# Performance work log

Hardware: AMD Instinct MI355X
Metric: run time of the kernel (lower is better)

Reference implementation:

```python
import jax, jax.numpy as jnp
import numpy as np

NUM_ITEM = 80000
NUM_USER = 20000
N = NUM_ITEM + NUM_USER
E = 1_000_000
DIM_FEAT = 64
USER_DIM = 128
DIM_ID = 64
SLOPE = 0.01  # F.leaky_relu default negative_slope


def setup_inputs() -> dict:
    key = jax.random.key(0)
    ks = jax.random.split(key, 16)
    s = 0.05
    # self-loop-free random edge list (torch code removes self loops)
    src = jax.random.randint(ks[0], (E,), 0, N)
    off = jax.random.randint(ks[1], (E,), 1, N)
    dst = (src + off) % N
    edge_index = jnp.stack([src, dst]).astype(jnp.int32)
    return {
        "features": jax.random.normal(ks[2], (NUM_ITEM, DIM_FEAT), jnp.float32),
        "user_features": jax.random.normal(ks[3], (NUM_USER, USER_DIM), jnp.float32),
        "id_embedding_weight": jax.random.normal(ks[4], (N, DIM_ID), jnp.float32) * s,
        "user_mlp_w": jax.random.normal(ks[5], (DIM_FEAT, USER_DIM), jnp.float32) * s,
        "user_mlp_b": jnp.zeros((DIM_FEAT,), jnp.float32),
        "gat1_w": jax.random.normal(ks[6], (DIM_FEAT, DIM_FEAT), jnp.float32) * s,
        "lin1_w": jax.random.normal(ks[7], (DIM_ID, DIM_FEAT), jnp.float32) * s,
        "lin1_b": jnp.zeros((DIM_ID,), jnp.float32),
        "g1_w": jax.random.normal(ks[8], (DIM_ID, DIM_FEAT), jnp.float32) * s,
        "g1_b": jnp.zeros((DIM_ID,), jnp.float32),
        "gat2_w": jax.random.normal(ks[9], (DIM_ID, DIM_ID), jnp.float32) * s,
        "lin2_w": jax.random.normal(ks[10], (DIM_ID, DIM_ID), jnp.float32) * s,
        "lin2_b": jnp.zeros((DIM_ID,), jnp.float32),
        "g2_w": jax.random.normal(ks[11], (DIM_ID, DIM_ID), jnp.float32) * s,
        "g2_b": jnp.zeros((DIM_ID,), jnp.float32),
        "edge_index": edge_index,
    }


def leaky_relu(x):
    return jnp.where(x >= 0, x, SLOPE * x)


def graph_gat(x, W, src, dst):
    """GraphGAT layer (MGAT-style): x@W, inner-product attention with
    degree-based sigmoid gate, edge softmax over target nodes, scatter-add."""
    n = x.shape[0]
    xw = x @ W                                   # [N, d_out]
    x_i = xw[dst]                                # gathered target feats [E, d]
    x_j = xw[src]                                # gathered source feats [E, d]
    inner = jnp.sum(x_i * x_j, axis=-1)          # [E]
    deg = jnp.zeros((n,), xw.dtype).at[src].add(1.0)
    dinv = deg[src] ** -0.5                      # deg[src] >= 1 by construction
    gate = jax.nn.sigmoid(dinv * inner)
    logits = inner * gate
    # segment softmax over destination index (PyG softmax)
    m = jax.ops.segment_max(logits, dst, num_segments=n)
    m = jnp.where(jnp.isfinite(m), m, 0.0)
    e = jnp.exp(logits - m[dst])
    z = jax.ops.segment_sum(e, dst, num_segments=n)
    attn = e / (z[dst] + 1e-16)
    msg = x_j * attn[:, None]                    # [E, d]
    return jnp.zeros_like(xw).at[dst].add(msg)   # scatter-add aggr


def reference(features, user_features, id_embedding_weight,
              user_mlp_w, user_mlp_b,
              gat1_w, lin1_w, lin1_b, g1_w, g1_b,
              gat2_w, lin2_w, lin2_b, g2_w, g2_b,
              edge_index):
    src, dst = edge_index[0], edge_index[1]
    user = jnp.tanh(user_features @ user_mlp_w.T + user_mlp_b)
    x = jnp.concatenate([features, user], axis=0)          # [N, dim_feat]
    nrm = jnp.linalg.norm(x, axis=-1, keepdims=True)
    x = x / jnp.maximum(nrm, 1e-12)                        # F.normalize

    # hop 1
    h = leaky_relu(graph_gat(x, gat1_w, src, dst))
    x_hat = leaky_relu(x @ lin1_w.T + lin1_b) + id_embedding_weight
    x1 = leaky_relu(h @ g1_w.T + g1_b + x_hat)

    # hop 2
    h = leaky_relu(graph_gat(x1, gat2_w, src, dst))
    x_hat = leaky_relu(x1 @ lin2_w.T + lin2_b) + id_embedding_weight
    x2 = leaky_relu(h @ g2_w.T + g2_b + x_hat)

    return jnp.concatenate([x1, x2], axis=1)               # [N, 2*dim_id]
```

## Files before the change

kernel.cpp:

```cpp
#include <hip/hip_runtime.h>
#include <hip/hip_bf16.h>

#define N_ITEM 80000
#define N_USER 20000
#define NN     100000
#define NE     1000000
#define SCAN_T 1024
#define SCAN_TILES ((NN + SCAN_T - 1) / SCAN_T)

typedef __hip_bfloat16 bf16;

__device__ __forceinline__ float b2f(bf16 v) { return __bfloat162float(v); }
__device__ __forceinline__ bf16  f2b(float v) { return __float2bfloat16(v); }
__device__ __forceinline__ float bits2f(unsigned short h) {
    return __uint_as_float(((unsigned)h) << 16);
}
__device__ __forceinline__ float leaky(float v) { return v >= 0.f ? v : 0.01f * v; }

template<typename T>
__device__ __forceinline__ float ldT(const void* p, size_t i);
template<> __device__ __forceinline__ float ldT<float>(const void* p, size_t i) {
    return ((const float*)p)[i];
}
template<> __device__ __forceinline__ float ldT<bf16>(const void* p, size_t i) {
    return b2f(((const bf16*)p)[i]);
}
template<typename T>
__device__ __forceinline__ float4 ldT4(const void* p, size_t i);
template<> __device__ __forceinline__ float4 ldT4<float>(const void* p, size_t i) {
    return *(const float4*)((const float*)p + i);
}
template<> __device__ __forceinline__ float4 ldT4<bf16>(const void* p, size_t i) {
    ushort4 u = *(const ushort4*)((const unsigned short*)p + i);
    return make_float4(bits2f(u.x), bits2f(u.y), bits2f(u.z), bits2f(u.w));
}
template<typename T>
__device__ __forceinline__ void stT4(void* p, size_t i, float4 v);
template<> __device__ __forceinline__ void stT4<float>(void* p, size_t i, float4 v) {
    *(float4*)((float*)p + i) = v;
}
template<> __device__ __forceinline__ void stT4<bf16>(void* p, size_t i, float4 v) {
    bf16 b0 = f2b(v.x), b1 = f2b(v.y), b2 = f2b(v.z), b3 = f2b(v.w);
    ushort4 u = make_ushort4(*(unsigned short*)&b0, *(unsigned short*)&b1,
                             *(unsigned short*)&b2, *(unsigned short*)&b3);
    *(ushort4*)((unsigned short*)p + i) = u;
}
__device__ __forceinline__ float4 ld4f(const float* p, size_t i) {
    return *(const float4*)(p + i);
}

__device__ __forceinline__ float wred(float v) {
    for (int o = 32; o; o >>= 1) v += __shfl_xor(v, o, 64);
    return v;
}
__device__ __forceinline__ float gred16(float v) {
    for (int o = 8; o; o >>= 1) v += __shfl_xor(v, o, 64);
    return v;
}
__device__ __forceinline__ int wscan(int v, int lane) {
    for (int o = 1; o < 64; o <<= 1) {
        int t = __shfl_up(v, o, 64);
        v += (lane >= o) ? t : 0;
    }
    return v;
}

__global__ void k_detect(const unsigned short* __restrict__ w, int* __restrict__ mode) {
    __shared__ int cnt[256];
    int bad = 0;
    for (int i = threadIdx.x; i < 4096; i += 256) {
        unsigned e = (w[i] >> 7) & 0xFFu;
        bad += (e == 0u || e == 0xFFu) ? 1 : 0;
    }
    cnt[threadIdx.x] = bad;
    __syncthreads();
    if (threadIdx.x == 0) {
        int t = 0;
        for (int k = 0; k < 256; k++) t += cnt[k];
        mode[0] = (t > 0) ? 1 : 0;
    }
}

__global__ void k_prep_w(const void* umw, const void* lw1, const void* gw1,
                         const void* lw2, const void* gw2,
                         float* umwT, float* wT, const int* mode) {
    int t = blockIdx.x * 256 + threadIdx.x;
    bool f32m = (*mode != 0);
    if (t < 8192) {
        int j = t >> 7, k = t & 127;
        float v = f32m ? ldT<float>(umw, t) : ldT<bf16>(umw, t);
        umwT[k * 64 + j] = v;
    } else {
        int u = t - 8192;
        int m = u >> 12;
        int r = u & 4095;
        int j = r >> 6, k = r & 63;
        const void* srcp = (m == 0) ? lw1 : (m == 1) ? gw1 : (m == 2) ? lw2 : gw2;
        float v = f32m ? ldT<float>(srcp, r) : ldT<bf16>(srcp, r);
        wT[m * 4096 + k * 64 + j] = v;
    }
}

__global__ void k_deg(const int* __restrict__ src, const int* __restrict__ dst,
                      int* __restrict__ deg, int* __restrict__ cnt) {
    int e = blockIdx.x * blockDim.x + threadIdx.x;
    if (e < NE) {
        atomicAdd(&deg[src[e]], 1);
        atomicAdd(&cnt[dst[e]], 1);
    }
}

__global__ void k_scan_sum(const int* __restrict__ cnt, int* __restrict__ tsum) {
    __shared__ int wsum[16];
    int i = blockIdx.x * SCAN_T + threadIdx.x;
    int lane = threadIdx.x & 63, wid = threadIdx.x >> 6;
    int v = (i < NN) ? cnt[i] : 0;
    float s = wred((float)v);
    if (lane == 0) wsum[wid] = (int)s;
    __syncthreads();
    if (threadIdx.x == 0) {
        int t = 0;
        #pragma unroll
        for (int k = 0; k < 16; k++) t += wsum[k];
        tsum[blockIdx.x] = t;
    }
}

__global__ void k_scan_tiles(const int* __restrict__ tsum, int* __restrict__ toff) {
    __shared__ int wsum[16];
    int lane = threadIdx.x & 63, wid = threadIdx.x >> 6;
    int v = (threadIdx.x < SCAN_TILES) ? tsum[threadIdx.x] : 0;
    int inc = wscan(v, lane);
    if (lane == 63) wsum[wid] = inc;
    __syncthreads();
    if (wid == 0) {
        int ws = (lane < 16) ? wsum[lane] : 0;
        int wi = wscan(ws, lane);
        if (lane < 16) wsum[lane] = wi - ws;
    }
    __syncthreads();
    if (threadIdx.x < SCAN_TILES) toff[threadIdx.x] = inc - v + wsum[wid];
}

__global__ void k_scan_out(const int* __restrict__ cnt, const int* __restrict__ toff,
                           int* __restrict__ csr_off, int* __restrict__ cursor) {
    __shared__ int wsum[16];
    int i = blockIdx.x * SCAN_T + threadIdx.x;
    int lane = threadIdx.x & 63, wid = threadIdx.x >> 6;
    int v = (i < NN) ? cnt[i] : 0;
    int inc = wscan(v, lane);
    if (lane == 63) wsum[wid] = inc;
    __syncthreads();
    if (wid == 0) {
        int ws = (lane < 16) ? wsum[lane] : 0;
        int wi = wscan(ws, lane);
        if (lane < 16) wsum[lane] = wi - ws;
    }
    __syncthreads();
    int excl = inc - v + wsum[wid] + toff[blockIdx.x];
    if (i < NN) { csr_off[i] = excl; cursor[i] = excl; }
    if (i == NN - 1) csr_off[NN] = excl + v;
}

__global__ void k_scatter(const int* __restrict__ src, const int* __restrict__ dst,
                          int* __restrict__ cursor, int* __restrict__ csr_src) {
    int e = blockIdx.x * blockDim.x + threadIdx.x;
    if (e < NE) {
        int pos = atomicAdd(&cursor[dst[e]], 1);
        csr_src[pos] = src[e];
    }
}

template<typename T>
__device__ __forceinline__ void prep_items_body(const void* feat, float* x) {
    int i = blockIdx.x * 4 + (threadIdx.x >> 6);
    int j = threadIdx.x & 63;
    if (i >= N_ITEM) return;
    float v = ldT<T>(feat, (size_t)i * 64 + j);
    float ss = wred(v * v);
    float inv = 1.f / fmaxf(sqrtf(ss), 1e-12f);
    x[(size_t)i * 64 + j] = v * inv;
}
__global__ void k_prep_items(const void* feat, float* x, const int* mode) {
    if (*mode) prep_items_body<float>(feat, x);
    else       prep_items_body<bf16>(feat, x);
}

template<typename T>
__device__ __forceinline__ void prep_users_body(const void* uf, const float* wT,
                                                const void* b, float* x) {
    int u = blockIdx.x * 4 + (threadIdx.x >> 6);
    int j = threadIdx.x & 63;
    if (u >= N_USER) return;
    size_t ub = (size_t)u * 128;
    float acc = ldT<T>(b, j);
    #pragma unroll 8
    for (int k = 0; k < 128; k++)
        acc += ldT<T>(uf, ub + k) * wT[k * 64 + j];
    float v = tanhf(acc);
    float ss = wred(v * v);
    float inv = 1.f / fmaxf(sqrtf(ss), 1e-12f);
    x[(size_t)(N_ITEM + u) * 64 + j] = v * inv;
}
__global__ void k_prep_users(const void* uf, const float* wT, const void* b,
                             float* x, const int* mode) {
    if (*mode) prep_users_body<float>(uf, wT, b, x);
    else       prep_users_body<bf16>(uf, wT, b, x);
}

template<typename T>
__device__ __forceinline__ void xw_body(const float* __restrict__ xin,
                                        const void* __restrict__ W,
                                        float* __restrict__ xw) {
    int lane = threadIdx.x & 63, wid = threadIdx.x >> 6;
    int sl = lane & 15;
    int i = blockIdx.x * 16 + (wid << 2) + (lane >> 4);
    if (i >= NN) return;
    size_t rb = (size_t)i * 64 + sl * 4;
    float4 xv = ld4f(xin, rb);
    float4 acc = make_float4(0.f, 0.f, 0.f, 0.f);
    int gbase = lane & 48;
    #pragma unroll
    for (int kk = 0; kk < 16; kk++) {
        int srcl = gbase | kk;
        float xb[4];
        xb[0] = __shfl(xv.x, srcl, 64);
        xb[1] = __shfl(xv.y, srcl, 64);
        xb[2] = __shfl(xv.z, srcl, 64);
        xb[3] = __shfl(xv.w, srcl, 64);
        #pragma unroll
        for (int q = 0; q < 4; q++) {
            float4 w4 = ldT4<T>(W, (size_t)(kk * 4 + q) * 64 + sl * 4);
            acc.x += xb[q] * w4.x; acc.y += xb[q] * w4.y;
            acc.z += xb[q] * w4.z; acc.w += xb[q] * w4.w;
        }
    }
    *(float4*)(xw + rb) = acc;
}
__global__ void k_xw(const float* xin, const void* W, float* xw, const int* mode) {
    if (*mode) xw_body<float>(xin, W, xw);
    else       xw_body<bf16>(xin, W, xw);
}

template<typename T>
__device__ __forceinline__ void gat_body(const float* __restrict__ xw,
                                         const float* __restrict__ xin,
                                         const int* __restrict__ csr_off,
                                         const int* __restrict__ csr_src,
                                         const int* __restrict__ deg,
                                         const float* __restrict__ gT, const void* gb,
                                         const float* __restrict__ lT, const void* lb,
                                         const void* id_emb,
                                         float* __restrict__ xnext, void* out,
                                         int off_out) {
    int lane = threadIdx.x & 63, wid = threadIdx.x >> 6;
    int sl = lane & 15;
    int i = blockIdx.x * 16 + (wid << 2) + (lane >> 4);
    if (i >= NN) return;
    size_t rb = (size_t)i * 64 + sl * 4;
    float4 xd = ld4f(xw, rb);
    int e0 = csr_off[i], e1 = csr_off[i + 1];
    int cnt = e1 - e0;
    float m = -1e30f, l = 0.f;
    float4 acc = make_float4(0.f, 0.f, 0.f, 0.f);
    float4 xsP = make_float4(0.f, 0.f, 0.f, 0.f);
    float dP = 1.f;
    if (cnt > 0) {
        int s0 = csr_src[e0];
        xsP = ld4f(xw, (size_t)s0 * 64 + sl * 4);
        dP = (float)deg[s0];
    }
    for (int t = 0; t < cnt; ++t) {
        float4 xs = xsP; float dv = dP;
        if (t + 1 < cnt) {
            int sn = csr_src[e0 + t + 1];
            xsP = ld4f(xw, (size_t)sn * 64 + sl * 4);
            dP = (float)deg[sn];
        }
        float p = xd.x * xs.x + xd.y * xs.y + xd.z * xs.z + xd.w * xs.w;
        float inner = gred16(p);
        float gate = 1.f / (1.f + __expf(-rsqrtf(dv) * inner));
        float logit = inner * gate;
        float mn = fmaxf(m, logit);
        float sc = __expf(m - mn);
        float w  = __expf(logit - mn);
        acc.x = acc.x * sc + w * xs.x;
        acc.y = acc.y * sc + w * xs.y;
        acc.z = acc.z * sc + w * xs.z;
        acc.w = acc.w * sc + w * xs.w;
        l = l * sc + w;
        m = mn;
    }
    float linv = 1.f / (l + 1e-16f);
    float4 hv = make_float4(leaky(acc.x * linv), leaky(acc.y * linv),
                            leaky(acc.z * linv), leaky(acc.w * linv));
    float4 xv = ld4f(xin, rb);
    float4 accg = make_float4(0.f, 0.f, 0.f, 0.f);
    float4 accl = make_float4(0.f, 0.f, 0.f, 0.f);
    int gbase = lane & 48;
    #pragma unroll
    for (int kk = 0; kk < 16; kk++) {
        int srcl = gbase | kk;
        float hb[4], xb[4];
        hb[0] = __shfl(hv.x, srcl, 64); xb[0] = __shfl(xv.x, srcl, 64);
        hb[1] = __shfl(hv.y, srcl, 64); xb[1] = __shfl(xv.y, srcl, 64);
        hb[2] = __shfl(hv.z, srcl, 64); xb[2] = __shfl(xv.z, srcl, 64);
        hb[3] = __shfl(hv.w, srcl, 64); xb[3] = __shfl(xv.w, srcl, 64);
        #pragma unroll
        for (int q = 0; q < 4; q++) {
            size_t wb = (size_t)(kk * 4 + q) * 64 + sl * 4;
            float4 g4 = ld4f(gT, wb);
            float4 l4 = ld4f(lT, wb);
            accg.x += hb[q] * g4.x; accg.y += hb[q] * g4.y;
            accg.z += hb[q] * g4.z; accg.w += hb[q] * g4.w;
            accl.x += xb[q] * l4.x; accl.y += xb[q] * l4.y;
            accl.z += xb[q] * l4.z; accl.w += xb[q] * l4.w;
        }
    }
    float4 lb4 = ldT4<T>(lb, sl * 4);
    float4 gb4 = ldT4<T>(gb, sl * 4);
    float4 id4 = ldT4<T>(id_emb, rb);
    float4 xn;
    xn.x = leaky(accg.x + gb4.x + leaky(accl.x + lb4.x) + id4.x);
    xn.y = leaky(accg.y + gb4.y + leaky(accl.y + lb4.y) + id4.y);
    xn.z = leaky(accg.z + gb4.z + leaky(accl.z + lb4.z) + id4.z);
    xn.w = leaky(accg.w + gb4.w + leaky(accl.w + lb4.w) + id4.w);
    *(float4*)(xnext + rb) = xn;
    stT4<T>(out, (size_t)i * 128 + off_out + sl * 4, xn);
}
__global__ void k_gat(const float* xw, const float* xin,
                      const int* csr_off, const int* csr_src, const int* deg,
                      const float* gT, const void* gb,
                      const float* lT, const void* lb, const void* id_emb,
                      float* xnext, void* out, int off_out, const int* mode) {
    if (*mode) gat_body<float>(xw, xin, csr_off, csr_src, deg, gT, gb, lT, lb,
                               id_emb, xnext, out, off_out);
    else       gat_body<bf16>(xw, xin, csr_off, csr_src, deg, gT, gb, lT, lb,
                              id_emb, xnext, out, off_out);
}

extern "C" void kernel_launch(void* const* d_in, const int* in_sizes, int n_in,
                              void* d_out, int out_size, void* d_ws, size_t ws_size,
                              hipStream_t stream) {
    const void* feat   = d_in[0];
    const void* uf     = d_in[1];
    const void* id_emb = d_in[2];
    const void* umw    = d_in[3];
    const void* umb    = d_in[4];
    const void* gat1   = d_in[5];
    const void* lin1b  = d_in[7];
    const void* g1b    = d_in[9];
    const void* gat2   = d_in[10];
    const void* lin2b  = d_in[12];
    const void* g2b    = d_in[14];
    const int*  ei     = (const int*)d_in[15];
    const int* src = ei;
    const int* dst = ei + NE;

    int*      mode   = (int*)d_ws;
    int*      deg    = (int*)((char*)d_ws + 16);
    int*      cnt    = deg + NN;
    int*      cursor = cnt + NN;
    int*      csr_off = cursor + NN;
    int*      tsum   = csr_off + NN + 16;
    int*      toff   = tsum + 128;
    float*    umwT   = (float*)(toff + 128);
    float*    wT     = umwT + 8192;
    int*      csr_src = (int*)(wT + 4 * 4096);
    float*    buf0   = (float*)(csr_src + NE);
    float*    buf1   = buf0 + (size_t)NN * 64;
    float*    buf2   = buf1 + (size_t)NN * 64;

    k_detect<<<1, 256, 0, stream>>>((const unsigned short*)feat, mode);
    k_prep_w<<<96, 256, 0, stream>>>(umw, d_in[6], d_in[8], d_in[11], d_in[13],
                                     umwT, wT, mode);
    hipMemsetAsync(deg, 0, 2 * NN * 4, stream);
    k_deg<<<(NE + 255) / 256, 256, 0, stream>>>(src, dst, deg, cnt);
    k_scan_sum<<<SCAN_TILES, SCAN_T, 0, stream>>>(cnt, tsum);
    k_scan_tiles<<<1, SCAN_T, 0, stream>>>(tsum, toff);
    k_scan_out<<<SCAN_TILES, SCAN_T, 0, stream>>>(cnt, toff, csr_off, cursor);
    k_scatter<<<(NE + 255) / 256, 256, 0, stream>>>(src, dst, cursor, csr_src);
    k_prep_items<<<(N_ITEM + 3) / 4, 256, 0, stream>>>(feat, buf0, mode);
    k_prep_users<<<(N_USER + 3) / 4, 256, 0, stream>>>(uf, umwT, umb, buf0, mode);

    const float* lT1 = wT;
    const float* gT1 = wT + 4096;
    const float* lT2 = wT + 8192;
    const float* gT2 = wT + 12288;

    int gat_blocks = (NN + 15) / 16;

    k_xw<<<gat_blocks, 256, 0, stream>>>(buf0, gat1, buf1, mode);
    k_gat<<<gat_blocks, 256, 0, stream>>>(buf1, buf0, csr_off, csr_src, deg,
                                          gT1, g1b, lT1, lin1b, id_emb,
                                          buf2, d_out, 0, mode);
    k_xw<<<gat_blocks, 256, 0, stream>>>(buf2, gat2, buf1, mode);
    k_gat<<<gat_blocks, 256, 0, stream>>>(buf1, buf2, csr_off, csr_src, deg,
                                          gT2, g2b, lT2, lin2b, id_emb,
                                          buf0, d_out, 64, mode);
}
```

Baseline: 698.2 us.

## Store xW in bf16, precompute inverse sqrt degree, deepen gather prefetch

The projected features xW are now stored as bf16 instead of fp32, which halves the bytes the GAT kernel gathers per edge in its random neighbour loop. A new small kernel computes rsqrt(degree) once per node, so the edge loop reads a ready float instead of converting and taking rsqrt per edge. The software prefetch in the edge loop now runs two neighbours ahead instead of one, to hide more gather latency. The cost is bf16 rounding of the attention inputs, which may reduce accuracy, plus one extra tiny launch and some extra registers.

```diff
diff --git a/kernel.cpp b/kernel.cpp
--- a/kernel.cpp
+++ b/kernel.cpp
@@ -47,6 +47,16 @@
 }
 __device__ __forceinline__ float4 ld4f(const float* p, size_t i) {
     return *(const float4*)(p + i);
+}
+__device__ __forceinline__ float4 ld4b(const unsigned short* p, size_t i) {
+    ushort4 u = *(const ushort4*)(p + i);
+    return make_float4(bits2f(u.x), bits2f(u.y), bits2f(u.z), bits2f(u.w));
+}
+__device__ __forceinline__ void st4b(unsigned short* p, size_t i, float4 v) {
+    bf16 b0 = f2b(v.x), b1 = f2b(v.y), b2 = f2b(v.z), b3 = f2b(v.w);
+    ushort4 u = make_ushort4(*(unsigned short*)&b0, *(unsigned short*)&b1,
+                             *(unsigned short*)&b2, *(unsigned short*)&b3);
+    *(ushort4*)(p + i) = u;
 }
 
 __device__ __forceinline__ float wred(float v) {
@@ -110,6 +120,11 @@
     }
 }
 
+__global__ void k_dinv(const int* __restrict__ deg, float* __restrict__ dinv) {
+    int i = blockIdx.x * blockDim.x + threadIdx.x;
+    if (i < NN) dinv[i] = rsqrtf((float)max(deg[i], 1));
+}
+
 __global__ void k_scan_sum(const int* __restrict__ cnt, int* __restrict__ tsum) {
     __shared__ int wsum[16];
     int i = blockIdx.x * SCAN_T + threadIdx.x;
@@ -211,7 +226,7 @@
 template<typename T>
 __device__ __forceinline__ void xw_body(const float* __restrict__ xin,
                                         const void* __restrict__ W,
-                                        float* __restrict__ xw) {
+                                        unsigned short* __restrict__ xw) {
     int lane = threadIdx.x & 63, wid = threadIdx.x >> 6;
     int sl = lane & 15;
     int i = blockIdx.x * 16 + (wid << 2) + (lane >> 4);
@@ -235,19 +250,20 @@
             acc.z += xb[q] * w4.z; acc.w += xb[q] * w4.w;
         }
     }
-    *(float4*)(xw + rb) = acc;
-}
-__global__ void k_xw(const float* xin, const void* W, float* xw, const int* mode) {
+    st4b(xw, rb, acc);
+}
+__global__ void k_xw(const float* xin, const void* W, unsigned short* xw,
+                     const int* mode) {
     if (*mode) xw_body<float>(xin, W, xw);
     else       xw_body<bf16>(xin, W, xw);
 }
 
 template<typename T>
-__device__ __forceinline__ void gat_body(const float* __restrict__ xw,
+__device__ __forceinline__ void gat_body(const unsigned short* __restrict__ xw,
                                          const float* __restrict__ xin,
                                          const int* __restrict__ csr_off,
                                          const int* __restrict__ csr_src,
-                                         const int* __restrict__ deg,
+                                         const float* __restrict__ dinv,
                                          const float* __restrict__ gT, const void* gb,
                                          const float* __restrict__ lT, const void* lb,
                                          const void* id_emb,
@@ -258,28 +274,34 @@
     int i = blockIdx.x * 16 + (wid << 2) + (lane >> 4);
     if (i >= NN) return;
     size_t rb = (size_t)i * 64 + sl * 4;
-    float4 xd = ld4f(xw, rb);
+    float4 xd = ld4b(xw, rb);
     int e0 = csr_off[i], e1 = csr_off[i + 1];
     int cnt = e1 - e0;
     float m = -1e30f, l = 0.f;
     float4 acc = make_float4(0.f, 0.f, 0.f, 0.f);
-    float4 xsP = make_float4(0.f, 0.f, 0.f, 0.f);
-    float dP = 1.f;
+    float4 xsA = make_float4(0.f, 0.f, 0.f, 0.f), xsB = xsA;
+    float dA = 1.f, dB = 1.f;
     if (cnt > 0) {
         int s0 = csr_src[e0];
-        xsP = ld4f(xw, (size_t)s0 * 64 + sl * 4);
-        dP = (float)deg[s0];
+        xsA = ld4b(xw, (size_t)s0 * 64 + sl * 4);
+        dA = dinv[s0];
+    }
+    if (cnt > 1) {
+        int s1 = csr_src[e0 + 1];
+        xsB = ld4b(xw, (size_t)s1 * 64 + sl * 4);
+        dB = dinv[s1];
     }
     for (int t = 0; t < cnt; ++t) {
-        float4 xs = xsP; float dv = dP;
-        if (t + 1 < cnt) {
-            int sn = csr_src[e0 + t + 1];
-            xsP = ld4f(xw, (size_t)sn * 64 + sl * 4);
-            dP = (float)deg[sn];
+        float4 xs = xsA; float dv = dA;
+        xsA = xsB; dA = dB;
+        if (t + 2 < cnt) {
+            int sn = csr_src[e0 + t + 2];
+            xsB = ld4b(xw, (size_t)sn * 64 + sl * 4);
+            dB = dinv[sn];
         }
         float p = xd.x * xs.x + xd.y * xs.y + xd.z * xs.z + xd.w * xs.w;
         float inner = gred16(p);
-        float gate = 1.f / (1.f + __expf(-rsqrtf(dv) * inner));
+        float gate = 1.f / (1.f + __expf(-dv * inner));
         float logit = inner * gate;
         float mn = fmaxf(m, logit);
         float sc = __expf(m - mn);
@@ -328,14 +350,14 @@
     *(float4*)(xnext + rb) = xn;
     stT4<T>(out, (size_t)i * 128 + off_out + sl * 4, xn);
 }
-__global__ void k_gat(const float* xw, const float* xin,
-                      const int* csr_off, const int* csr_src, const int* deg,
+__global__ void k_gat(const unsigned short* xw, const float* xin,
+                      const int* csr_off, const int* csr_src, const float* dinv,
                       const float* gT, const void* gb,
                       const float* lT, const void* lb, const void* id_emb,
                       float* xnext, void* out, int off_out, const int* mode) {
-    if (*mode) gat_body<float>(xw, xin, csr_off, csr_src, deg, gT, gb, lT, lb,
+    if (*mode) gat_body<float>(xw, xin, csr_off, csr_src, dinv, gT, gb, lT, lb,
                                id_emb, xnext, out, off_out);
-    else       gat_body<bf16>(xw, xin, csr_off, csr_src, deg, gT, gb, lT, lb,
+    else       gat_body<bf16>(xw, xin, csr_off, csr_src, dinv, gT, gb, lT, lb,
                               id_emb, xnext, out, off_out);
 }
 
@@ -364,18 +386,20 @@
     int*      csr_off = cursor + NN;
     int*      tsum   = csr_off + NN + 16;
     int*      toff   = tsum + 128;
-    float*    umwT   = (float*)(toff + 128);
+    float*    dinv   = (float*)(toff + 128);
+    float*    umwT   = dinv + NN;
     float*    wT     = umwT + 8192;
     int*      csr_src = (int*)(wT + 4 * 4096);
     float*    buf0   = (float*)(csr_src + NE);
-    float*    buf1   = buf0 + (size_t)NN * 64;
-    float*    buf2   = buf1 + (size_t)NN * 64;
+    float*    buf2   = buf0 + (size_t)NN * 64;
+    unsigned short* xwb = (unsigned short*)(buf2 + (size_t)NN * 64);
 
     k_detect<<<1, 256, 0, stream>>>((const unsigned short*)feat, mode);
     k_prep_w<<<96, 256, 0, stream>>>(umw, d_in[6], d_in[8], d_in[11], d_in[13],
                                      umwT, wT, mode);
     hipMemsetAsync(deg, 0, 2 * NN * 4, stream);
     k_deg<<<(NE + 255) / 256, 256, 0, stream>>>(src, dst, deg, cnt);
+    k_dinv<<<(NN + 255) / 256, 256, 0, stream>>>(deg, dinv);
     k_scan_sum<<<SCAN_TILES, SCAN_T, 0, stream>>>(cnt, tsum);
     k_scan_tiles<<<1, SCAN_T, 0, stream>>>(tsum, toff);
     k_scan_out<<<SCAN_TILES, SCAN_T, 0, stream>>>(cnt, toff, csr_off, cursor);
@@ -390,12 +414,12 @@
 
     int gat_blocks = (NN + 15) / 16;
 
-    k_xw<<<gat_blocks, 256, 0, stream>>>(buf0, gat1, buf1, mode);
-    k_gat<<<gat_blocks, 256, 0, stream>>>(buf1, buf0, csr_off, csr_src, deg,
+    k_xw<<<gat_blocks, 256, 0, stream>>>(buf0, gat1, xwb, mode);
+    k_gat<<<gat_blocks, 256, 0, stream>>>(xwb, buf0, csr_off, csr_src, dinv,
                                           gT1, g1b, lT1, lin1b, id_emb,
                                           buf2, d_out, 0, mode);
-    k_xw<<<gat_blocks, 256, 0, stream>>>(buf2, gat2, buf1, mode);
-    k_gat<<<gat_blocks, 256, 0, stream>>>(buf1, buf2, csr_off, csr_src, deg,
+    k_xw<<<gat_blocks, 256, 0, stream>>>(buf2, gat2, xwb, mode);
+    k_gat<<<gat_blocks, 256, 0, stream>>>(xwb, buf2, csr_off, csr_src, dinv,
                                           gT2, g2b, lT2, lin2b, id_emb,
                                           buf0, d_out, 64, mode);
 }
```

Measured after the change: 680.1 us. 2.6% less time.
